# Kernel optimization log

Measured on AMD Instinct MI355X. Metric: run time of the kernel, lower is better.

## Reference

```python
import jax, jax.numpy as jnp
import numpy as np

N_NODES = 50000


def _gcn_conv(x, edge_index, W, b):
    # PyG GCNConv (default flags): add self-loops, symmetric normalization,
    # linear transform, scatter-add aggregation, bias.
    N = x.shape[0]
    row, col = edge_index[0], edge_index[1]  # messages flow row -> col
    loop = jnp.arange(N)
    row_f = jnp.concatenate([row, loop])
    col_f = jnp.concatenate([col, loop])
    deg = jax.ops.segment_sum(jnp.ones(col_f.shape[0], dtype=x.dtype), col_f,
                              num_segments=N)
    deg_inv_sqrt = jnp.where(deg > 0, jax.lax.rsqrt(jnp.maximum(deg, 1e-12)), 0.0)
    norm = deg_inv_sqrt[row_f] * deg_inv_sqrt[col_f]  # [E+N]
    h = x @ W                                          # [N, out]
    msg = h[row_f] * norm[:, None]                     # gather + scale
    out = jax.ops.segment_sum(msg, col_f, num_segments=N)  # scatter-add
    return out + b


def setup_inputs() -> dict:
    key = jax.random.key(0)
    ks = jax.random.split(key, 6)
    d_in, d_hid, d_out = 128, 128, 64
    E = 800000
    x = jax.random.normal(ks[0], (N_NODES, d_in), dtype=jnp.float32)
    edge_index = jax.random.randint(ks[1], (2, E), 0, N_NODES, dtype=jnp.int64)
    edge_label = jax.random.uniform(ks[2], (100000,), dtype=jnp.float32)
    edge_label_index = jax.random.randint(ks[3], (2, 100000), 0, N_NODES,
                                          dtype=jnp.int64)
    # Glorot-style init for GCNConv linear weights
    W1 = jax.random.normal(ks[4], (d_in, d_hid), dtype=jnp.float32) / np.sqrt(d_in)
    b1 = jnp.zeros((d_hid,), dtype=jnp.float32)
    W2 = jax.random.normal(ks[5], (d_hid, d_out), dtype=jnp.float32) / np.sqrt(d_hid)
    b2 = jnp.zeros((d_out,), dtype=jnp.float32)
    return {"x": x, "edge_index": edge_index, "edge_label": edge_label,
            "edge_label_index": edge_label_index,
            "W1": W1, "b1": b1, "W2": W2, "b2": b2}


def reference(x, edge_index, edge_label, edge_label_index, W1, b1, W2, b2):
    h = jax.nn.relu(_gcn_conv(x, edge_index, W1, b1))
    # dropout is identity in eval mode (training=False)
    z = _gcn_conv(h, edge_index, W2, b2)
    return z
```

## Files before the change

kernel.cpp:

```cpp
#include <hip/hip_runtime.h>


typedef unsigned int u32;
typedef unsigned short ushort;
typedef __attribute__((ext_vector_type(8))) short short8;
typedef __attribute__((ext_vector_type(8))) unsigned short us8;
typedef __attribute__((ext_vector_type(4))) float floatx4;

static inline int cdiv_l(long a, int b) { return (int)((a + b - 1) / b); }

constexpr int NPB  = 512;
constexpr int EPB  = 4096;
constexpr int MAXB = 128;
constexpr int CAP  = 12288;

__device__ __forceinline__ u32 pack_bf16(float a, float b) {
  union { float f; u32 i; } ua, ub;
  ua.f = a; ub.f = b;
  u32 x = (ua.i + 0x7fffu + ((ua.i >> 16) & 1u)) >> 16;
  u32 y = (ub.i + 0x7fffu + ((ub.i >> 16) & 1u)) & 0xffff0000u;
  return x | y;
}

__device__ __forceinline__ short bf16r(float f) {
  union { float f; u32 i; } u; u.f = f;
  return (short)((u.i + 0x7fffu + ((u.i >> 16) & 1u)) >> 16);
}

__device__ __forceinline__ void dq8(float* a, uint2 v, float sd) {
  a[0] += (float)(v.x & 255u) * sd;
  a[1] += (float)((v.x >> 8) & 255u) * sd;
  a[2] += (float)((v.x >> 16) & 255u) * sd;
  a[3] += (float)(v.x >> 24) * sd;
  a[4] += (float)(v.y & 255u) * sd;
  a[5] += (float)((v.y >> 8) & 255u) * sd;
  a[6] += (float)((v.y >> 16) & 255u) * sd;
  a[7] += (float)(v.y >> 24) * sd;
}

__global__ __launch_bounds__(256) void k_pack(
    const float* __restrict__ W1, const float* __restrict__ W2,
    u32* __restrict__ w1f, u32* __restrict__ w2f, int* __restrict__ cur) {
  const int tid = threadIdx.x;
  const int b = blockIdx.x;
  if (b == 0 && tid < MAXB) cur[tid] = 0;
  if (b < 8) {
    const int s = b * 256 + tid;
    const int lane = s & 63, frag = s >> 6;
    const int kc = frag >> 3, cb = frag & 7;
    const float* src =
        W1 + (long)(kc * 32 + (lane >> 4) * 8) * 128 + cb * 16 + (lane & 15);
    u32 o[4];
#pragma unroll
    for (int p = 0; p < 4; ++p)
      o[p] = pack_bf16(src[(2 * p) * 128], src[(2 * p + 1) * 128]);
    *(uint4*)(w1f + (long)s * 4) = make_uint4(o[0], o[1], o[2], o[3]);
  } else {
    const int s = (b - 8) * 256 + tid;
    const int lane = s & 63, frag = s >> 6;
    const int kc = frag >> 2, cb = frag & 3;
    const float* src =
        W2 + (long)(kc * 32 + (lane >> 4) * 8) * 64 + cb * 16 + (lane & 15);
    u32 o[4];
#pragma unroll
    for (int p = 0; p < 4; ++p)
      o[p] = pack_bf16(src[(2 * p) * 64], src[(2 * p + 1) * 64]);
    *(uint4*)(w2f + (long)s * 4) = make_uint4(o[0], o[1], o[2], o[3]);
  }
}

__global__ __launch_bounds__(256) void k_fused1(
    const int* __restrict__ ei, int* __restrict__ cur, u32* __restrict__ ebuf,
    int E, int NBE,
    const float* __restrict__ x, const u32* __restrict__ w1f,
    u32* __restrict__ h8, float* __restrict__ scale, int N) {
  __shared__ float eb[4][16 * 133];
  const int tid = threadIdx.x;

  if (blockIdx.x < (unsigned)NBE) {
    u32* ecache = (u32*)&eb[0][0];
    int* hist   = (int*)&eb[2][0];
    int* curs   = hist + MAXB;
    const int* ecol = ei + E;
    if (tid < MAXB) hist[tid] = 0;
    __syncthreads();
    const int base = blockIdx.x * EPB;
#pragma unroll
    for (int j = 0; j < EPB / 256; ++j) {
      int e = base + j * 256 + tid;
      u32 pk = 0xffffffffu;
      if (e < E) {
        u32 r = (u32)ei[e];
        u32 c = (u32)ecol[e];
        pk = r | (c << 16);
        atomicAdd(hist + (c >> 9), 1);
      }
      ecache[j * 256 + tid] = pk;
    }
    __syncthreads();
    if (tid < MAXB) {
      int n = hist[tid];
      curs[tid] = tid * CAP + (n ? atomicAdd(cur + tid, n) : 0);
    }
    __syncthreads();
#pragma unroll
    for (int j = 0; j < EPB / 256; ++j) {
      u32 pk = ecache[j * 256 + tid];
      if (pk != 0xffffffffu) {
        u32 c = pk >> 16;
        int b = c >> 9;
        int p = atomicAdd(curs + b, 1);
        if (p < (b + 1) * CAP)
          ebuf[p] = (pk & 0xffffu) | ((c & (NPB - 1)) << 16);
      }
    }
    return;
  }

  constexpr int K = 128, NC = 8, LROW = 133;
  const int w = tid >> 6, lane = tid & 63;
  const int quad = lane >> 4, n16 = lane & 15;
  const int row0 = ((blockIdx.x - NBE) * 4 + w) * 16;

  floatx4 acc[NC];
#pragma unroll
  for (int c = 0; c < NC; ++c) acc[c] = {0.f, 0.f, 0.f, 0.f};

  const int am = row0 + n16;
  const bool av = am < N;
  const float* arow = x + (long)am * K;
  const short8* wf = (const short8*)w1f;

#pragma unroll
  for (int kc = 0; kc < 4; ++kc) {
    const int kb = kc * 32 + quad * 8;
    float4 a0 = make_float4(0.f, 0.f, 0.f, 0.f);
    float4 a1 = make_float4(0.f, 0.f, 0.f, 0.f);
    if (av) {
      a0 = *(const float4*)(arow + kb);
      a1 = *(const float4*)(arow + kb + 4);
    }
    short8 af;
    af[0] = bf16r(a0.x); af[1] = bf16r(a0.y); af[2] = bf16r(a0.z); af[3] = bf16r(a0.w);
    af[4] = bf16r(a1.x); af[5] = bf16r(a1.y); af[6] = bf16r(a1.z); af[7] = bf16r(a1.w);
#pragma unroll
    for (int c = 0; c < NC; ++c) {
      short8 bf = wf[(kc * 8 + c) * 64 + lane];
      acc[c] = __builtin_amdgcn_mfma_f32_16x16x32_bf16(af, bf, acc[c], 0, 0, 0);
    }
  }

  float* ep = eb[w];
#pragma unroll
  for (int c = 0; c < NC; ++c)
#pragma unroll
    for (int r = 0; r < 4; ++r)
      ep[(quad * 4 + r) * LROW + c * 16 + n16] = acc[c][r];
  __syncthreads();

  const int rr = lane >> 2, seg = lane & 3;
  const float* rowp = ep + rr * LROW + seg * 32;
  float m = 0.f;
#pragma unroll
  for (int c = 0; c < 32; ++c) m = fmaxf(m, fabsf(rowp[c]));
  m = fmaxf(m, __shfl_xor(m, 1, 4));
  m = fmaxf(m, __shfl_xor(m, 2, 4));
  const float inv = (m > 0.f) ? 127.f / m : 0.f;
  const float s = m / 127.f;
  u32 q[8];
#pragma unroll
  for (int wd = 0; wd < 8; ++wd) {
    u32 b0 = (u32)((int)rintf(rowp[wd * 4 + 0] * inv) + 128);
    u32 b1 = (u32)((int)rintf(rowp[wd * 4 + 1] * inv) + 128);
    u32 b2 = (u32)((int)rintf(rowp[wd * 4 + 2] * inv) + 128);
    u32 b3 = (u32)((int)rintf(rowp[wd * 4 + 3] * inv) + 128);
    q[wd] = (b0 & 255u) | ((b1 & 255u) << 8) | ((b2 & 255u) << 16) | (b3 << 24);
  }
  const int rg = row0 + rr;
  if (rg < N) {
    uint4* dst = (uint4*)(h8 + (long)rg * 32 + seg * 8);
    dst[0] = make_uint4(q[0], q[1], q[2], q[3]);
    dst[1] = make_uint4(q[4], q[5], q[6], q[7]);
    if (seg == 0) scale[rg] = s;
  }
}

__global__ __launch_bounds__(NPB) void k_csr(const u32* __restrict__ ebuf,
                                             const int* __restrict__ cur,
                                             const float* __restrict__ scale,
                                             int* __restrict__ off,
                                             int* __restrict__ deg,
                                             float* __restrict__ dis,
                                             float* __restrict__ sd,
                                             ushort* __restrict__ csr, int N) {
  __shared__ int cnt[NPB];
  __shared__ int curl[NPB];
  __shared__ int wsum[NPB / 64];
  const int tid = threadIdx.x;
  const int b = blockIdx.x;
  const int s = b * CAP;
  const int e = s + min(cur[b], CAP);
  cnt[tid] = 0;
  __syncthreads();
  for (int i = s + tid; i < e; i += NPB)
    atomicAdd(cnt + (ebuf[i] >> 16), 1);
  __syncthreads();
  const int lane = tid & 63, w = tid >> 6;
  const int v = cnt[tid];
  const int vp = (v + 7) & ~7;
  int incl = vp;
#pragma unroll
  for (int d = 1; d < 64; d <<= 1) {
    int x = __shfl_up(incl, d, 64);
    if (lane >= d) incl += x;
  }
  if (lane == 63) wsum[w] = incl;
  __syncthreads();
  if (w == 0 && lane < NPB / 64) {
    int sv = wsum[lane];
#pragma unroll
    for (int d = 1; d < NPB / 64; d <<= 1) {
      int x = __shfl_up(sv, d, 64);
      if (lane >= d) sv += x;
    }
    wsum[lane] = sv;
  }
  __syncthreads();
  int excl = ((w > 0) ? wsum[w - 1] : 0) + incl - vp;
  int node = b * NPB + tid;
  if (node < N) {
    float dv = rsqrtf((float)v + 1.0f);
    off[node] = s + excl;
    deg[node] = v;
    dis[node] = dv;
    sd[node] = scale[node] * dv;
  }
  curl[tid] = excl;
  __syncthreads();
  for (int i = s + tid; i < e; i += NPB) {
    u32 pk = ebuf[i];
    int p = atomicAdd(curl + (pk >> 16), 1);
    csr[s + p] = (ushort)(pk & 0xffffu);
  }
}

__global__ __launch_bounds__(256) void k_gg(
    const uint2* __restrict__ h8, const int* __restrict__ off,
    const int* __restrict__ deg, const ushort* __restrict__ csr,
    const float* __restrict__ dis, const float* __restrict__ sd,
    const float* __restrict__ b1, const u32* __restrict__ w2f,
    u32* __restrict__ h2, float* __restrict__ s2, int N) {
  constexpr int LG = 65;
  constexpr int LC = 66;
  __shared__ u32 lg[16 * LG];
  __shared__ float cb[16 * LC];
  const int tid = threadIdx.x;
  const int r = tid >> 4;
  const int lf = tid & 15;
  const int row0 = blockIdx.x * 16;
  const int n = row0 + r;

  u32 gw[4] = {0, 0, 0, 0};
  if (n < N) {
    const int s = off[n], e = s + deg[n];
    const float dn = dis[n];
    float acc[8] = {};
    float K = 0.f;
    {
      float sn = sd[n];
      dq8(acc, h8[(long)n * 16 + lf], sn);
      K += sn;
    }
    int j = s;
    for (; j + 8 <= e; j += 8) {
      us8 ev = *(const us8*)(csr + j);
      const int i0 = ev[0], i1 = ev[1], i2 = ev[2], i3 = ev[3];
      const int i4 = ev[4], i5 = ev[5], i6 = ev[6], i7 = ev[7];
      const float d0 = sd[i0], d1 = sd[i1], d2 = sd[i2], d3 = sd[i3];
      const float d4 = sd[i4], d5 = sd[i5], d6 = sd[i6], d7 = sd[i7];
      uint2 v0 = h8[(long)i0 * 16 + lf];
      uint2 v1 = h8[(long)i1 * 16 + lf];
      uint2 v2 = h8[(long)i2 * 16 + lf];
      uint2 v3 = h8[(long)i3 * 16 + lf];
      uint2 v4 = h8[(long)i4 * 16 + lf];
      uint2 v5 = h8[(long)i5 * 16 + lf];
      uint2 v6 = h8[(long)i6 * 16 + lf];
      uint2 v7 = h8[(long)i7 * 16 + lf];
      dq8(acc, v0, d0); dq8(acc, v1, d1); dq8(acc, v2, d2); dq8(acc, v3, d3);
      dq8(acc, v4, d4); dq8(acc, v5, d5); dq8(acc, v6, d6); dq8(acc, v7, d7);
      K += ((d0 + d1) + (d2 + d3)) + ((d4 + d5) + (d6 + d7));
    }
    if (j < e) {
      us8 ev = *(const us8*)(csr + j);
#pragma unroll
      for (int t = 0; t < 8; ++t) {
        if (j + t < e) {
          const int it = ev[t];
          const float dt = sd[it];
          dq8(acc, h8[(long)it * 16 + lf], dt);
          K += dt;
        }
      }
    }
    const int f8 = lf * 8;
    const float4 bv0 = *(const float4*)(b1 + f8);
    const float4 bv1 = *(const float4*)(b1 + f8 + 4);
    const float bb[8] = {bv0.x, bv0.y, bv0.z, bv0.w, bv1.x, bv1.y, bv1.z, bv1.w};
    const float kc = 128.f * K;
#pragma unroll
    for (int q = 0; q < 8; ++q)
      acc[q] = fmaxf((acc[q] - kc) * dn + bb[q], 0.f);
#pragma unroll
    for (int q = 0; q < 4; ++q)
      gw[q] = pack_bf16(acc[2 * q], acc[2 * q + 1]);
  }
#pragma unroll
  for (int q = 0; q < 4; ++q) lg[r * LG + lf * 4 + q] = gw[q];
  __syncthreads();

  const int w = tid >> 6, lane = tid & 63;
  const int quad = lane >> 4, n16 = lane & 15;
  floatx4 acc4 = {0.f, 0.f, 0.f, 0.f};
#pragma unroll
  for (int kc = 0; kc < 4; ++kc) {
    const int kb = kc * 32 + quad * 8;
    const u32* ap = &lg[n16 * LG + (kb >> 1)];
    u32 aw[4] = {ap[0], ap[1], ap[2], ap[3]};
    short8 af = *(short8*)aw;
    short8 bf = ((const short8*)w2f)[(kc * 4 + w) * 64 + lane];
    acc4 = __builtin_amdgcn_mfma_f32_16x16x32_bf16(af, bf, acc4, 0, 0, 0);
  }
  float dd[4];
#pragma unroll
  for (int r4 = 0; r4 < 4; ++r4) {
    int rg = row0 + quad * 4 + r4;
    dd[r4] = (rg < N) ? dis[rg] : 0.f;
  }
#pragma unroll
  for (int r4 = 0; r4 < 4; ++r4)
    cb[(quad * 4 + r4) * LC + w * 16 + n16] = acc4[r4] * dd[r4];
  __syncthreads();

  const int rr2 = tid >> 4, lf2 = tid & 15;
  const float* rp = cb + rr2 * LC + lf2 * 4;
  float mx = fmaxf(fmaxf(fabsf(rp[0]), fabsf(rp[1])),
                   fmaxf(fabsf(rp[2]), fabsf(rp[3])));
  mx = fmaxf(mx, __shfl_xor(mx, 1, 16));
  mx = fmaxf(mx, __shfl_xor(mx, 2, 16));
  mx = fmaxf(mx, __shfl_xor(mx, 4, 16));
  mx = fmaxf(mx, __shfl_xor(mx, 8, 16));
  const float inv2 = (mx > 0.f) ? 127.f / mx : 0.f;
  const int rg2 = row0 + rr2;
  if (rg2 < N) {
    u32 q0 = (u32)((int)rintf(rp[0] * inv2) + 128);
    u32 q1 = (u32)((int)rintf(rp[1] * inv2) + 128);
    u32 q2 = (u32)((int)rintf(rp[2] * inv2) + 128);
    u32 q3 = (u32)((int)rintf(rp[3] * inv2) + 128);
    h2[(long)rg2 * 16 + lf2] =
        (q0 & 255u) | ((q1 & 255u) << 8) | ((q2 & 255u) << 16) | (q3 << 24);
    if (lf2 == 0) s2[rg2] = mx / 127.f;
  }
}

__global__ __launch_bounds__(256) void k_gather2(
    const uint2* __restrict__ hs, const int* __restrict__ off,
    const int* __restrict__ deg, const ushort* __restrict__ csr,
    const float* __restrict__ dis, const float* __restrict__ sc2,
    const float* __restrict__ bias, float* __restrict__ out, int N) {
  constexpr int L = 8;
  const int local = threadIdx.x / L;
  const int lf = threadIdx.x % L;
  const int n = blockIdx.x * (256 / L) + local;
  if (n >= N) return;
  const int s = off[n], e = s + deg[n];
  float acc[8] = {};
  float K = 0.f;
  {
    float t0 = sc2[n];
    dq8(acc, hs[(long)n * L + lf], t0);
    K += t0;
  }
  int j = s;
  for (; j + 8 <= e; j += 8) {
    us8 ev = *(const us8*)(csr + j);
    const int i0 = ev[0], i1 = ev[1], i2 = ev[2], i3 = ev[3];
    const int i4 = ev[4], i5 = ev[5], i6 = ev[6], i7 = ev[7];
    const float d0 = sc2[i0], d1 = sc2[i1], d2 = sc2[i2], d3 = sc2[i3];
    const float d4 = sc2[i4], d5 = sc2[i5], d6 = sc2[i6], d7 = sc2[i7];
    uint2 v0 = hs[(long)i0 * L + lf];
    uint2 v1 = hs[(long)i1 * L + lf];
    uint2 v2 = hs[(long)i2 * L + lf];
    uint2 v3 = hs[(long)i3 * L + lf];
    uint2 v4 = hs[(long)i4 * L + lf];
    uint2 v5 = hs[(long)i5 * L + lf];
    uint2 v6 = hs[(long)i6 * L + lf];
    uint2 v7 = hs[(long)i7 * L + lf];
    dq8(acc, v0, d0); dq8(acc, v1, d1); dq8(acc, v2, d2); dq8(acc, v3, d3);
    dq8(acc, v4, d4); dq8(acc, v5, d5); dq8(acc, v6, d6); dq8(acc, v7, d7);
    K += ((d0 + d1) + (d2 + d3)) + ((d4 + d5) + (d6 + d7));
  }
  if (j < e) {
    us8 ev = *(const us8*)(csr + j);
#pragma unroll
    for (int t = 0; t < 8; ++t) {
      if (j + t < e) {
        const int it = ev[t];
        const float dt = sc2[it];
        dq8(acc, hs[(long)it * L + lf], dt);
        K += dt;
      }
    }
  }
  const float d = dis[n];
  const float kc = 128.f * K;
  const int f8 = lf * 8;
  const float4 b0 = *(const float4*)(bias + f8);
  const float4 b1v = *(const float4*)(bias + f8 + 4);
  float4 o0, o1;
  o0.x = (acc[0] - kc) * d + b0.x;
  o0.y = (acc[1] - kc) * d + b0.y;
  o0.z = (acc[2] - kc) * d + b0.z;
  o0.w = (acc[3] - kc) * d + b0.w;
  o1.x = (acc[4] - kc) * d + b1v.x;
  o1.y = (acc[5] - kc) * d + b1v.y;
  o1.z = (acc[6] - kc) * d + b1v.z;
  o1.w = (acc[7] - kc) * d + b1v.w;
  *(float4*)(out + (long)n * 64 + f8) = o0;
  *(float4*)(out + (long)n * 64 + f8 + 4) = o1;
}

extern "C" void kernel_launch(void* const* d_in, const int* in_sizes, int n_in,
                              void* d_out, int out_size, void* d_ws, size_t ws_size,
                              hipStream_t stream) {
  const float* x  = (const float*)d_in[0];
  const int*   ei = (const int*)d_in[1];
  const float* W1 = (const float*)d_in[4];
  const float* b1 = (const float*)d_in[5];
  const float* W2 = (const float*)d_in[6];
  const float* b2 = (const float*)d_in[7];
  float* out = (float*)d_out;

  const int N = in_sizes[0] / 128;
  const int E = in_sizes[1] / 2;
  const int NBKT = cdiv_l(N, NPB);
  const int NBE  = cdiv_l(E, EPB);
  const int G1   = cdiv_l(N, 64);

  const long Np = (N + 64) & ~63L;
  const long BW = (long)NBKT * CAP;
  int*    cur   = (int*)d_ws;
  int*    off   = cur + 128;
  int*    deg   = off + Np;
  float*  dis   = (float*)(deg + Np);
  float*  scale = dis + Np;
  float*  sd    = scale + Np;
  float*  s2    = sd + Np;
  u32*    w1f   = (u32*)(s2 + Np);
  u32*    w2f   = w1f + 8192;
  u32*    ebuf  = w2f + 4096;
  ushort* csr   = (ushort*)(ebuf + BW);
  u32*    h8    = (u32*)(csr + BW);
  u32*    h2    = h8 + (long)N * 32;

  k_pack<<<12, 256, 0, stream>>>(W1, W2, w1f, w2f, cur);

  k_fused1<<<NBE + G1, 256, 0, stream>>>(ei, cur, ebuf, E, NBE, x, w1f, h8,
                                         scale, N);

  k_csr<<<NBKT, NPB, 0, stream>>>(ebuf, cur, scale, off, deg, dis, sd, csr, N);

  k_gg<<<cdiv_l(N, 16), 256, 0, stream>>>((const uint2*)h8, off, deg, csr,
                                          dis, sd, b1, w2f, h2, s2, N);

  k_gather2<<<cdiv_l(N, 32), 256, 0, stream>>>((const uint2*)h2, off, deg, csr,
                                               dis, s2, b2, out, N);
}
```

Baseline: 152.1 us.

## Fold weight packing into fused kernel; pack W1 into LDS per block

Removes the separate k_pack launch. Each GEMM block now converts W1 to bf16 directly into shared memory in the MFMA fragment layout, and extra blocks appended to k_fused1 pack W2 to global memory. The bucket cursors are cleared with a memset instead of by the pack kernel. This saves a launch and a dependency, at the cost of every GEMM block redundantly reading and converting all of W1 and an extra barrier before reusing LDS.

```diff
diff --git a/kernel.cpp b/kernel.cpp
--- a/kernel.cpp
+++ b/kernel.cpp
@@ -38,25 +38,18 @@
   a[7] += (float)(v.y >> 24) * sd;
 }
 
-__global__ __launch_bounds__(256) void k_pack(
-    const float* __restrict__ W1, const float* __restrict__ W2,
-    u32* __restrict__ w1f, u32* __restrict__ w2f, int* __restrict__ cur) {
+__global__ __launch_bounds__(256) void k_fused1(
+    const int* __restrict__ ei, int* __restrict__ cur, u32* __restrict__ ebuf,
+    int E, int NBE, int G1,
+    const float* __restrict__ x, const float* __restrict__ W1,
+    const float* __restrict__ W2, u32* __restrict__ w2f,
+    u32* __restrict__ h8, float* __restrict__ scale, int N) {
+  __shared__ float eb[4][16 * 133];
   const int tid = threadIdx.x;
-  const int b = blockIdx.x;
-  if (b == 0 && tid < MAXB) cur[tid] = 0;
-  if (b < 8) {
-    const int s = b * 256 + tid;
-    const int lane = s & 63, frag = s >> 6;
-    const int kc = frag >> 3, cb = frag & 7;
-    const float* src =
-        W1 + (long)(kc * 32 + (lane >> 4) * 8) * 128 + cb * 16 + (lane & 15);
-    u32 o[4];
-#pragma unroll
-    for (int p = 0; p < 4; ++p)
-      o[p] = pack_bf16(src[(2 * p) * 128], src[(2 * p + 1) * 128]);
-    *(uint4*)(w1f + (long)s * 4) = make_uint4(o[0], o[1], o[2], o[3]);
-  } else {
-    const int s = (b - 8) * 256 + tid;
+  const int blk = blockIdx.x;
+
+  if (blk >= NBE + G1) {
+    const int s = (blk - NBE - G1) * 256 + tid;
     const int lane = s & 63, frag = s >> 6;
     const int kc = frag >> 2, cb = frag & 3;
     const float* src =
@@ -66,25 +59,17 @@
     for (int p = 0; p < 4; ++p)
       o[p] = pack_bf16(src[(2 * p) * 64], src[(2 * p + 1) * 64]);
     *(uint4*)(w2f + (long)s * 4) = make_uint4(o[0], o[1], o[2], o[3]);
-  }
-}
-
-__global__ __launch_bounds__(256) void k_fused1(
-    const int* __restrict__ ei, int* __restrict__ cur, u32* __restrict__ ebuf,
-    int E, int NBE,
-    const float* __restrict__ x, const u32* __restrict__ w1f,
-    u32* __restrict__ h8, float* __restrict__ scale, int N) {
-  __shared__ float eb[4][16 * 133];
-  const int tid = threadIdx.x;
-
-  if (blockIdx.x < (unsigned)NBE) {
+    return;
+  }
+
+  if (blk < NBE) {
     u32* ecache = (u32*)&eb[0][0];
     int* hist   = (int*)&eb[2][0];
     int* curs   = hist + MAXB;
     const int* ecol = ei + E;
     if (tid < MAXB) hist[tid] = 0;
     __syncthreads();
-    const int base = blockIdx.x * EPB;
+    const int base = blk * EPB;
 #pragma unroll
     for (int j = 0; j < EPB / 256; ++j) {
       int e = base + j * 256 + tid;
@@ -117,10 +102,25 @@
     return;
   }
 
-  constexpr int K = 128, NC = 8, LROW = 133;
+  constexpr int NC = 8, LROW = 133;
+  ushort* wl = (ushort*)&eb[0][0];
+  for (int i = tid; i < 4096; i += 256) {
+    float4 v = ((const float4*)W1)[i];
+    const int base = i << 2;
+    const int k = base >> 7, m = base & 127;
+    const int slot =
+        ((k >> 5) * 8 + (m >> 4)) * 64 + ((k >> 3) & 3) * 16 + (m & 15);
+    const int s8 = slot * 8 + (k & 7);
+    wl[s8]      = (ushort)bf16r(v.x);
+    wl[s8 + 8]  = (ushort)bf16r(v.y);
+    wl[s8 + 16] = (ushort)bf16r(v.z);
+    wl[s8 + 24] = (ushort)bf16r(v.w);
+  }
+  __syncthreads();
+
   const int w = tid >> 6, lane = tid & 63;
   const int quad = lane >> 4, n16 = lane & 15;
-  const int row0 = ((blockIdx.x - NBE) * 4 + w) * 16;
+  const int row0 = ((blk - NBE) * 4 + w) * 16;
 
   floatx4 acc[NC];
 #pragma unroll
@@ -128,8 +128,8 @@
 
   const int am = row0 + n16;
   const bool av = am < N;
-  const float* arow = x + (long)am * K;
-  const short8* wf = (const short8*)w1f;
+  const float* arow = x + (long)am * 128;
+  const short8* wf = (const short8*)wl;
 
 #pragma unroll
   for (int kc = 0; kc < 4; ++kc) {
@@ -149,6 +149,7 @@
       acc[c] = __builtin_amdgcn_mfma_f32_16x16x32_bf16(af, bf, acc[c], 0, 0, 0);
     }
   }
+  __syncthreads();
 
   float* ep = eb[w];
 #pragma unroll
@@ -455,17 +456,16 @@
   float*  scale = dis + Np;
   float*  sd    = scale + Np;
   float*  s2    = sd + Np;
-  u32*    w1f   = (u32*)(s2 + Np);
-  u32*    w2f   = w1f + 8192;
+  u32*    w2f   = (u32*)(s2 + Np);
   u32*    ebuf  = w2f + 4096;
   ushort* csr   = (ushort*)(ebuf + BW);
   u32*    h8    = (u32*)(csr + BW);
   u32*    h2    = h8 + (long)N * 32;
 
-  k_pack<<<12, 256, 0, stream>>>(W1, W2, w1f, w2f, cur);
-
-  k_fused1<<<NBE + G1, 256, 0, stream>>>(ei, cur, ebuf, E, NBE, x, w1f, h8,
-                                         scale, N);
+  hipMemsetAsync(cur, 0, MAXB * sizeof(int), stream);
+
+  k_fused1<<<NBE + G1 + 4, 256, 0, stream>>>(ei, cur, ebuf, E, NBE, G1, x,
+                                             W1, W2, w2f, h8, scale, N);
 
   k_csr<<<NBKT, NPB, 0, stream>>>(ebuf, cur, scale, off, deg, dis, sd, csr, N);
 
```

Result: slower. 161.8 us (+6.4%).
